# Kernel optimization log

Hardware: AMD Instinct MI355X
Metric: run time of the kernel (lower is better)

## Reference

```python
import jax, jax.numpy as jnp
import numpy as np

B, N, K, H, W = 8, 64, 32, 256, 256


def setup_inputs() -> dict:
    key = jax.random.key(0)
    k1, k2, k3, k4, k5, k6 = jax.random.split(key, 6)
    original = jax.random.normal(k1, (B, 3, H, W), dtype=jnp.float32)
    # loc = (cx, cy, w, h) in normalized coords; keep w,h >= 0.05 so the
    # unnormalized gaussian stays finite.
    cxy = jax.random.uniform(k2, (B, N, 2), dtype=jnp.float32)
    wh = jax.random.uniform(k3, (B, N, 2), dtype=jnp.float32) * 0.45 + 0.05
    loc = jnp.concatenate([cxy, wh], axis=-1)
    masks = jax.random.normal(k4, (B, N, K), dtype=jnp.float32)
    proto = jax.random.normal(k5, (B, H, W, K), dtype=jnp.float32)
    conf = jax.random.uniform(k6, (B, N), dtype=jnp.float32)
    return {"original": original, "loc": loc, "masks": masks,
            "proto": proto, "conf": conf}


def _unnormal_gaussian(loc, h, w):
    # Unnormalized 2D axis-aligned gaussian per prior, evaluated on a
    # half-pixel normalized grid. loc: [B, N, 4] = (cx, cy, sx, sy).
    ys = (jnp.arange(h, dtype=loc.dtype) + 0.5) / h  # [H]
    xs = (jnp.arange(w, dtype=loc.dtype) + 0.5) / w  # [W]
    cx = loc[..., 0][:, :, None, None]
    cy = loc[..., 1][:, :, None, None]
    sx = loc[..., 2][:, :, None, None]
    sy = loc[..., 3][:, :, None, None]
    dy = (ys[None, None, :, None] - cy) / sy  # [B,N,H,1]
    dx = (xs[None, None, None, :] - cx) / sx  # [B,N,1,W]
    return jnp.exp(-0.5 * (dx * dx + dy * dy))  # [B,N,H,W]


def reference(original, loc, masks, proto, conf):
    b, c, h, w = original.shape
    gauss = _unnormal_gaussian(loc, h, w)  # [B,N,H,W]
    # lincomb: sigmoid(proto @ mask_coeffs^T) -> assembled instance masks
    assembled = jax.nn.sigmoid(jnp.einsum('bhwk,bnk->bnhw', proto, masks))
    attention = assembled * gauss                      # [B,N,H,W]
    mask_conf = attention * conf[:, :, None, None]     # einsum 'abcd,ab->abcd'
    denom = jnp.sum(mask_conf, axis=1, keepdims=True) + 1e-5
    final_conf = 1.0 - jnp.sum(mask_conf * mask_conf / denom, axis=1)  # [B,H,W]
    # F.interpolate(..., resizeShape, 'bilinear'): proto res == resizeShape,
    # so this is an identity bilinear resize (half-pixel convention).
    resized_conf = jax.image.resize(final_conf, (b, h, w), method='bilinear')
    total_conf = jnp.sum(resized_conf, axis=0)                        # [H,W]
    weighted_mean = jnp.einsum('bchw,bhw->chw', original, resized_conf)
    squared_diff = (original - weighted_mean) ** 2                    # [B,C,H,W]
    weighted_diff = squared_diff * resized_conf[:, None]  # 'abcd,acd->abcd'
    weighted_variance = weighted_diff / total_conf
    return jnp.sum(weighted_variance)
```

## Files before the change

### kernel.cpp

```cpp
#include <hip/hip_runtime.h>
#include <hip/hip_bf16.h>

#define NPIX 65536
#define NB 8
#define NN 64
#define KK 32
#define LOG2E 1.4426950408889634f

typedef __attribute__((ext_vector_type(4))) float f32x4;
typedef __attribute__((ext_vector_type(8))) short bf16x8;

__device__ __forceinline__ float rcpf(float x) { return __builtin_amdgcn_rcpf(x); }
__device__ __forceinline__ float exp2_fast(float x) { float r; asm("v_exp_f32 %0, %1" : "=v"(r) : "v"(x)); return r; }
__device__ __forceinline__ float log2_fast(float x) { float r; asm("v_log_f32 %0, %1" : "=v"(r) : "v"(x)); return r; }
__device__ __forceinline__ short f2bf(float x) {
    union { __hip_bfloat16 b; short s; } u; u.b = __float2bfloat16(x); return u.s;
}

__global__ __launch_bounds__(256) void k_phase1(
    const float* __restrict__ loc,
    const float* __restrict__ masks,
    const float* __restrict__ proto,
    const float* __restrict__ conf,
    float* __restrict__ fcb)
{
    __shared__ float4 sprm[2][NN];

    const int b    = blockIdx.x >> 7;
    const int rp   = blockIdx.x & 127;
    const int tid  = threadIdx.x;
    const int lane = tid & 63;
    const int wave = tid >> 6;
    const int nl   = lane & 15;
    const int kg   = lane >> 4;
    const int rw   = wave >> 1;
    const int half = wave & 1;
    const int row  = rp * 2 + rw;

    const float inv = 1.0f / 256.0f;

    if (tid < 128) {
        const int rr = tid >> 6, n = tid & 63;
        float4 L = ((const float4*)loc)[b * NN + n];
        float isx = rcpf(L.z), isy = rcpf(L.w);
        float gx = -0.72134752f * isx * isx;
        float gy = -0.72134752f * isy * isy;
        float fyr = (rp * 2 + rr + 0.5f) * inv;
        float dy  = fyr - L.y;
        float ey  = fmaf(dy * dy, gy, log2_fast(conf[b * NN + n]));
        float beta  = -2.0f * gx * L.x;
        float gamma = fmaf(gx * L.x, L.x, ey);
        sprm[rr][n] = make_float4(gx, beta, gamma, 0.f);
    }
    __syncthreads();

    int mi[4], ni[4];
    {
        bf16x8 Ap, Bp;
#pragma unroll
        for (int j = 0; j < 8; ++j) { Ap[j] = 0; Bp[j] = 0; }
        if (kg == 0) {
            Ap[0] = f2bf((float)nl);
            Ap[1] = f2bf(1.0f);
            Bp[0] = f2bf(1.0f);
            Bp[1] = f2bf((float)(16 * nl));
        }
        f32x4 z = {0.f, 0.f, 0.f, 0.f};
        f32x4 d = __builtin_amdgcn_mfma_f32_16x16x32_bf16(Ap, Bp, z, 0, 0, 0);
#pragma unroll
        for (int r = 0; r < 4; ++r) {
            int v = (int)(d[r] + 0.5f);
            mi[r] = v & 15;
            ni[r] = (v >> 4) & 15;
        }
    }
    const int ni0 = ni[0];

    bf16x8 Mf[4];
#pragma unroll
    for (int t = 0; t < 4; ++t) {
        const float* mp = masks + ((size_t)b * NN + 16 * t + nl) * KK + kg * 8;
        float4 u0 = *(const float4*)mp;
        float4 u1 = *(const float4*)(mp + 4);
        bf16x8 v;
        v[0] = f2bf(u0.x * -LOG2E); v[1] = f2bf(u0.y * -LOG2E);
        v[2] = f2bf(u0.z * -LOG2E); v[3] = f2bf(u0.w * -LOG2E);
        v[4] = f2bf(u1.x * -LOG2E); v[5] = f2bf(u1.y * -LOG2E);
        v[6] = f2bf(u1.z * -LOG2E); v[7] = f2bf(u1.w * -LOG2E);
        Mf[t] = v;
    }

    float Pa[4][4], Pb[4][4], Pc[4][4];
#pragma unroll
    for (int t = 0; t < 4; ++t)
#pragma unroll
        for (int r = 0; r < 4; ++r) {
            float4 P = sprm[rw][16 * t + mi[r]];
            Pa[t][r] = P.x; Pb[t][r] = P.y; Pc[t][r] = P.z;
        }

#define EVALT(ACC, T)                                                       \
    {                                                                       \
        _Pragma("unroll") for (int r = 0; r < 4; ++r) {                     \
            float e  = fmaf(fmaf(Pa[T][r], fx, Pb[T][r]), fx, Pc[T][r]);    \
            float aa = exp2_fast(e) * rcpf(1.0f + exp2_fast(ACC[r]));       \
            S1 += aa; S2 = fmaf(aa, aa, S2);                                \
        }                                                                   \
    }

    const size_t prow = (size_t)b * NPIX + (size_t)row * 256;
    const int pxb = half * 128;
    const float* pp0 = proto + (prow + pxb + nl) * KK + kg * 8;

    float4 c0 = *(const float4*)(pp0);
    float4 c1 = *(const float4*)(pp0 + 4);

#pragma unroll
    for (int i = 0; i < 8; ++i) {
        float4 n0, n1;
        if (i < 7) {
            const float* np = pp0 + (size_t)(i + 1) * 16 * KK;
            n0 = *(const float4*)np;
            n1 = *(const float4*)(np + 4);
        }

        bf16x8 Pf;
        Pf[0] = f2bf(c0.x); Pf[1] = f2bf(c0.y); Pf[2] = f2bf(c0.z); Pf[3] = f2bf(c0.w);
        Pf[4] = f2bf(c1.x); Pf[5] = f2bf(c1.y); Pf[6] = f2bf(c1.z); Pf[7] = f2bf(c1.w);

        f32x4 z = {0.f, 0.f, 0.f, 0.f};
        f32x4 acc0 = __builtin_amdgcn_mfma_f32_16x16x32_bf16(Mf[0], Pf, z, 0, 0, 0);
        f32x4 acc1 = __builtin_amdgcn_mfma_f32_16x16x32_bf16(Mf[1], Pf, z, 0, 0, 0);
        f32x4 acc2 = __builtin_amdgcn_mfma_f32_16x16x32_bf16(Mf[2], Pf, z, 0, 0, 0);
        f32x4 acc3 = __builtin_amdgcn_mfma_f32_16x16x32_bf16(Mf[3], Pf, z, 0, 0, 0);

        const float fx = (pxb + i * 16 + ni0 + 0.5f) * inv;
        float S1 = 0.f, S2 = 0.f;
        EVALT(acc0, 0);
        EVALT(acc1, 1);
        EVALT(acc2, 2);
        EVALT(acc3, 3);

        S1 += __shfl_xor(S1, 16); S1 += __shfl_xor(S1, 32);
        S2 += __shfl_xor(S2, 16); S2 += __shfl_xor(S2, 32);
        if (lane < 16)
            fcb[prow + pxb + i * 16 + ni0] = 1.0f - S2 * rcpf(S1 + 1e-5f);

        if (i < 7) { c0 = n0; c1 = n1; }
    }
#undef EVALT
}

__global__ __launch_bounds__(256) void k_phase2(
    const float* __restrict__ original,
    const float* __restrict__ fcb,
    float* __restrict__ out)
{
    const int pix = blockIdx.x * 256 + threadIdx.x;

    float f[NB];
    float tot = 0.f;
#pragma unroll
    for (int b = 0; b < NB; ++b) { f[b] = fcb[(size_t)b * NPIX + pix]; tot += f[b]; }

    float part = 0.f;
#pragma unroll
    for (int c = 0; c < 3; ++c) {
        float o[NB];
        float wm = 0.f;
#pragma unroll
        for (int b = 0; b < NB; ++b) {
            o[b] = original[((size_t)(b * 3 + c)) * NPIX + pix];
            wm = fmaf(o[b], f[b], wm);
        }
#pragma unroll
        for (int b = 0; b < NB; ++b) {
            float d = o[b] - wm;
            part = fmaf(d * d, f[b], part);
        }
    }
    part *= rcpf(tot);

#pragma unroll
    for (int off = 32; off > 0; off >>= 1) part += __shfl_down(part, off);
    __shared__ float sred[4];
    if ((threadIdx.x & 63) == 0) sred[threadIdx.x >> 6] = part;
    __syncthreads();
    if (threadIdx.x == 0) atomicAdd(out, sred[0] + sred[1] + sred[2] + sred[3]);
}

__global__ __launch_bounds__(256) void k_fused(
    const float* __restrict__ original, const float* __restrict__ loc,
    const float* __restrict__ masks, const float* __restrict__ proto,
    const float* __restrict__ conf, float* __restrict__ out)
{
    const int pix = blockIdx.x * 256 + threadIdx.x;
    const float inv = 1.0f / 256.0f;
    const float fx = ((pix & 255) + 0.5f) * inv;
    const float fy = ((pix >> 8) + 0.5f) * inv;

    float f[NB];
    for (int b = 0; b < NB; ++b) {
        const float4* p4 = (const float4*)(proto + ((size_t)b * NPIX + pix) * KK);
        const float4* m4 = (const float4*)(masks + (size_t)b * NN * KK);
        const float4* l4 = (const float4*)(loc + (size_t)b * NN * 4);
        const float*  cf = conf + b * NN;
        float S1 = 0.f, S2 = 0.f;
        for (int n = 0; n < NN; ++n) {
            float sa = 0.f;
#pragma unroll
            for (int j = 0; j < 8; ++j) {
                float4 A = p4[j], m = m4[n * 8 + j];
                sa = fmaf(A.w, m.w, fmaf(A.z, m.z, fmaf(A.y, m.y, fmaf(A.x, m.x, sa))));
            }
            const float4 L = l4[n];
            float isx = rcpf(L.z), isy = rcpf(L.w);
            float dx = (fx - L.x) * isx, dy = (fy - L.y) * isy;
            float g = __expf(-0.5f * fmaf(dx, dx, dy * dy));
            float a = g * rcpf(1.0f + __expf(-sa)) * cf[n];
            S1 += a;
            S2 = fmaf(a, a, S2);
        }
        f[b] = 1.0f - S2 * rcpf(S1 + 1e-5f);
    }
    float tot = 0.f;
#pragma unroll
    for (int b = 0; b < NB; ++b) tot += f[b];
    float part = 0.f;
#pragma unroll
    for (int c = 0; c < 3; ++c) {
        float o[NB];
        float wm = 0.f;
#pragma unroll
        for (int b = 0; b < NB; ++b) {
            o[b] = original[((size_t)(b * 3 + c)) * NPIX + pix];
            wm = fmaf(o[b], f[b], wm);
        }
#pragma unroll
        for (int b = 0; b < NB; ++b) {
            float d = o[b] - wm;
            part = fmaf(d * d, f[b], part);
        }
    }
    part *= rcpf(tot);

#pragma unroll
    for (int off = 32; off > 0; off >>= 1) part += __shfl_down(part, off);
    __shared__ float sred[4];
    if ((threadIdx.x & 63) == 0) sred[threadIdx.x >> 6] = part;
    __syncthreads();
    if (threadIdx.x == 0) atomicAdd(out, sred[0] + sred[1] + sred[2] + sred[3]);
}

extern "C" void kernel_launch(void* const* d_in, const int* in_sizes, int n_in,
                              void* d_out, int out_size, void* d_ws, size_t ws_size,
                              hipStream_t stream) {
    const float* original = (const float*)d_in[0];
    const float* loc      = (const float*)d_in[1];
    const float* masks    = (const float*)d_in[2];
    const float* proto    = (const float*)d_in[3];
    const float* conf     = (const float*)d_in[4];
    float* out = (float*)d_out;

    hipMemsetAsync(out, 0, sizeof(float), stream);

    const size_t fc_bytes = (size_t)NB * NPIX * sizeof(float);
    if (ws_size >= fc_bytes) {
        float* fcb = (float*)d_ws;
        k_phase1<<<NB * 128, 256, 0, stream>>>(loc, masks, proto, conf, fcb);
        k_phase2<<<NPIX / 256, 256, 0, stream>>>(original, fcb, out);
    } else {
        k_fused<<<NPIX / 256, 256, 0, stream>>>(original, loc, masks, proto, conf, out);
    }
}
```

Baseline: 35.56 us.

## Split phase1 into one row per block and batch cross-lane reductions

Phase1 now launches twice as many blocks, each handling a single image row, with each wave covering 64 pixels (4 iterations) instead of 128. The mask coefficient loads are issued before the gaussian parameter setup so their latency overlaps the barrier. The per-iteration shuffle reductions and stores are moved after the loop and batched, which lets the four reductions interleave. The intent is better occupancy and latency hiding, at the cost of recomputing per-block mask fragments and parameters for twice as many blocks.

After: 37.98 us. +6.8%, slower.

```diff
diff --git a/kernel.cpp b/kernel.cpp
--- a/kernel.cpp
+++ b/kernel.cpp
@@ -24,37 +24,41 @@
     const float* __restrict__ conf,
     float* __restrict__ fcb)
 {
-    __shared__ float4 sprm[2][NN];
-
-    const int b    = blockIdx.x >> 7;
-    const int rp   = blockIdx.x & 127;
+    __shared__ float4 sprm[NN];
+
+    const int b    = blockIdx.x >> 8;
+    const int row  = blockIdx.x & 255;
     const int tid  = threadIdx.x;
     const int lane = tid & 63;
     const int wave = tid >> 6;
     const int nl   = lane & 15;
     const int kg   = lane >> 4;
-    const int rw   = wave >> 1;
-    const int half = wave & 1;
-    const int row  = rp * 2 + rw;
 
     const float inv = 1.0f / 256.0f;
 
-    if (tid < 128) {
-        const int rr = tid >> 6, n = tid & 63;
-        float4 L = ((const float4*)loc)[b * NN + n];
+    float4 mu0[4], mu1[4];
+#pragma unroll
+    for (int t = 0; t < 4; ++t) {
+        const float* mp = masks + ((size_t)b * NN + 16 * t + nl) * KK + kg * 8;
+        mu0[t] = *(const float4*)mp;
+        mu1[t] = *(const float4*)(mp + 4);
+    }
+
+    if (tid < NN) {
+        float4 L = ((const float4*)loc)[b * NN + tid];
         float isx = rcpf(L.z), isy = rcpf(L.w);
         float gx = -0.72134752f * isx * isx;
         float gy = -0.72134752f * isy * isy;
-        float fyr = (rp * 2 + rr + 0.5f) * inv;
+        float fyr = (row + 0.5f) * inv;
         float dy  = fyr - L.y;
-        float ey  = fmaf(dy * dy, gy, log2_fast(conf[b * NN + n]));
+        float ey  = fmaf(dy * dy, gy, log2_fast(conf[b * NN + tid]));
         float beta  = -2.0f * gx * L.x;
         float gamma = fmaf(gx * L.x, L.x, ey);
-        sprm[rr][n] = make_float4(gx, beta, gamma, 0.f);
+        sprm[tid] = make_float4(gx, beta, gamma, 0.f);
     }
     __syncthreads();
 
-    int mi[4], ni[4];
+    int mi[4], ni0;
     {
         bf16x8 Ap, Bp;
 #pragma unroll
@@ -71,22 +75,18 @@
         for (int r = 0; r < 4; ++r) {
             int v = (int)(d[r] + 0.5f);
             mi[r] = v & 15;
-            ni[r] = (v >> 4) & 15;
-        }
-    }
-    const int ni0 = ni[0];
+            if (r == 0) ni0 = (v >> 4) & 15;
+        }
+    }
 
     bf16x8 Mf[4];
 #pragma unroll
     for (int t = 0; t < 4; ++t) {
-        const float* mp = masks + ((size_t)b * NN + 16 * t + nl) * KK + kg * 8;
-        float4 u0 = *(const float4*)mp;
-        float4 u1 = *(const float4*)(mp + 4);
         bf16x8 v;
-        v[0] = f2bf(u0.x * -LOG2E); v[1] = f2bf(u0.y * -LOG2E);
-        v[2] = f2bf(u0.z * -LOG2E); v[3] = f2bf(u0.w * -LOG2E);
-        v[4] = f2bf(u1.x * -LOG2E); v[5] = f2bf(u1.y * -LOG2E);
-        v[6] = f2bf(u1.z * -LOG2E); v[7] = f2bf(u1.w * -LOG2E);
+        v[0] = f2bf(mu0[t].x * -LOG2E); v[1] = f2bf(mu0[t].y * -LOG2E);
+        v[2] = f2bf(mu0[t].z * -LOG2E); v[3] = f2bf(mu0[t].w * -LOG2E);
+        v[4] = f2bf(mu1[t].x * -LOG2E); v[5] = f2bf(mu1[t].y * -LOG2E);
+        v[6] = f2bf(mu1[t].z * -LOG2E); v[7] = f2bf(mu1[t].w * -LOG2E);
         Mf[t] = v;
     }
 
@@ -95,7 +95,7 @@
     for (int t = 0; t < 4; ++t)
 #pragma unroll
         for (int r = 0; r < 4; ++r) {
-            float4 P = sprm[rw][16 * t + mi[r]];
+            float4 P = sprm[16 * t + mi[r]];
             Pa[t][r] = P.x; Pb[t][r] = P.y; Pc[t][r] = P.z;
         }
 
@@ -109,16 +109,18 @@
     }
 
     const size_t prow = (size_t)b * NPIX + (size_t)row * 256;
-    const int pxb = half * 128;
+    const int pxb = wave * 64;
     const float* pp0 = proto + (prow + pxb + nl) * KK + kg * 8;
+
+    float S1a[4], S2a[4];
 
     float4 c0 = *(const float4*)(pp0);
     float4 c1 = *(const float4*)(pp0 + 4);
 
 #pragma unroll
-    for (int i = 0; i < 8; ++i) {
+    for (int i = 0; i < 4; ++i) {
         float4 n0, n1;
-        if (i < 7) {
+        if (i < 3) {
             const float* np = pp0 + (size_t)(i + 1) * 16 * KK;
             n0 = *(const float4*)np;
             n1 = *(const float4*)(np + 4);
@@ -140,15 +142,27 @@
         EVALT(acc1, 1);
         EVALT(acc2, 2);
         EVALT(acc3, 3);
-
-        S1 += __shfl_xor(S1, 16); S1 += __shfl_xor(S1, 32);
-        S2 += __shfl_xor(S2, 16); S2 += __shfl_xor(S2, 32);
-        if (lane < 16)
-            fcb[prow + pxb + i * 16 + ni0] = 1.0f - S2 * rcpf(S1 + 1e-5f);
-
-        if (i < 7) { c0 = n0; c1 = n1; }
+        S1a[i] = S1; S2a[i] = S2;
+
+        if (i < 3) { c0 = n0; c1 = n1; }
     }
 #undef EVALT
+
+#pragma unroll
+    for (int i = 0; i < 4; ++i) {
+        S1a[i] += __shfl_xor(S1a[i], 16);
+        S2a[i] += __shfl_xor(S2a[i], 16);
+    }
+#pragma unroll
+    for (int i = 0; i < 4; ++i) {
+        S1a[i] += __shfl_xor(S1a[i], 32);
+        S2a[i] += __shfl_xor(S2a[i], 32);
+    }
+    if (lane < 16) {
+#pragma unroll
+        for (int i = 0; i < 4; ++i)
+            fcb[prow + pxb + i * 16 + ni0] = 1.0f - S2a[i] * rcpf(S1a[i] + 1e-5f);
+    }
 }
 
 __global__ __launch_bounds__(256) void k_phase2(
@@ -267,7 +281,7 @@
     const size_t fc_bytes = (size_t)NB * NPIX * sizeof(float);
     if (ws_size >= fc_bytes) {
         float* fcb = (float*)d_ws;
-        k_phase1<<<NB * 128, 256, 0, stream>>>(loc, masks, proto, conf, fcb);
+        k_phase1<<<NB * 256, 256, 0, stream>>>(loc, masks, proto, conf, fcb);
         k_phase2<<<NPIX / 256, 256, 0, stream>>>(original, fcb, out);
     } else {
         k_fused<<<NPIX / 256, 256, 0, stream>>>(original, loc, masks, proto, conf, out);
```
